# Performance work log

Measured on AMD Instinct MI355X. Metric: run time of the kernel, lower is better.

The kernel has to match this reference:

```python
import jax, jax.numpy as jnp
import numpy as np

N, E, G = 50000, 400000, 64   # nodes, edges, graphs
HEADS = 4
F_IN, H1, C3, OUT = 64, 96, 64, 10  # in feats, hidden (3*32), last conv out, classes


def seg_softmax(alpha, index, num_segments):
    # numerically stable softmax over segments (PyG softmax(alpha, edge_index_i))
    amax = jax.ops.segment_max(alpha, index, num_segments)
    amax = jnp.where(jnp.isfinite(amax), amax, 0.0)
    e = jnp.exp(alpha - amax[index])
    denom = jax.ops.segment_sum(e, index, num_segments)
    return e / (denom[index] + 1e-16)


def general_conv(x, src, dst, Wm, bm, att, Ws=None, bs=None):
    # GeneralConv (attention=True, additive, directed_msg, aggr='add')
    C = att.shape[-1]
    m = (x[src] @ Wm + bm).reshape(-1, HEADS, C)              # [E,H,C] gathered messages
    a = jax.nn.leaky_relu((m * att).sum(-1), 0.2)             # [E,H] attention logits
    a = seg_softmax(a, dst, N)                                # segment softmax per dest node
    agg = jax.ops.segment_sum(m * a[..., None], dst, N)       # [N,H,C] scatter-add
    out = agg.mean(axis=1)                                    # head mean -> [N,C]
    if Ws is None:                                            # lin_self = Identity (in==out)
        return out + x
    return out + x @ Ws + bs


def setup_inputs():
    key = jax.random.key(0)
    ks = jax.random.split(key, 16)
    s = 0.05
    return {
        "x": jax.random.normal(ks[0], (N, F_IN), jnp.float32),
        "edge_index": jax.random.randint(ks[1], (2, E), 0, N, jnp.int32),
        "batch": jnp.sort(jax.random.randint(ks[2], (N,), 0, G, jnp.int32)),
        # layer 1: F_IN -> H1
        "Wm1": jax.random.normal(ks[3], (F_IN, HEADS * H1), jnp.float32) * s,
        "bm1": jnp.zeros((HEADS * H1,), jnp.float32),
        "att1": jax.random.normal(ks[4], (HEADS, H1), jnp.float32) * s,
        "Ws1": jax.random.normal(ks[5], (F_IN, H1), jnp.float32) * s,
        "bs1": jnp.zeros((H1,), jnp.float32),
        # layer 2: H1 -> H1 (lin_self = Identity)
        "Wm2": jax.random.normal(ks[6], (H1, HEADS * H1), jnp.float32) * s,
        "bm2": jnp.zeros((HEADS * H1,), jnp.float32),
        "att2": jax.random.normal(ks[7], (HEADS, H1), jnp.float32) * s,
        # layer 3: H1 -> C3
        "Wm3": jax.random.normal(ks[8], (H1, HEADS * C3), jnp.float32) * s,
        "bm3": jnp.zeros((HEADS * C3,), jnp.float32),
        "att3": jax.random.normal(ks[9], (HEADS, C3), jnp.float32) * s,
        "Ws3": jax.random.normal(ks[10], (H1, C3), jnp.float32) * s,
        "bs3": jnp.zeros((C3,), jnp.float32),
        # classifier
        "Wfc": jax.random.normal(ks[11], (C3, OUT), jnp.float32) * s,
        "bfc": jnp.zeros((OUT,), jnp.float32),
    }


def reference(x, edge_index, batch, Wm1, bm1, att1, Ws1, bs1,
              Wm2, bm2, att2, Wm3, bm3, att3, Ws3, bs3, Wfc, bfc):
    src, dst = edge_index[0], edge_index[1]
    h = general_conv(x, src, dst, Wm1, bm1, att1, Ws1, bs1)
    h = general_conv(h, src, dst, Wm2, bm2, att2)
    h = general_conv(h, src, dst, Wm3, bm3, att3, Ws3, bs3)
    # global_mean_pool
    ssum = jax.ops.segment_sum(h, batch, G)
    cnt = jax.ops.segment_sum(jnp.ones((N, 1), h.dtype), batch, G)
    pooled = ssum / jnp.maximum(cnt, 1.0)                      # [G,C3]
    logits = pooled @ Wfc + bfc
    return jax.nn.log_softmax(logits, axis=1)
```

## Files before the change

kernel.cpp:

```cpp
#include <hip/hip_runtime.h>
#include <hip/hip_bf16.h>
#include <stdint.h>

using bf16 = __hip_bfloat16;
typedef __attribute__((ext_vector_type(8))) short bf16x8;
typedef __attribute__((ext_vector_type(4))) float f32x4;
typedef __attribute__((ext_vector_type(2))) float f32x2;

#define NN 50000
#define NE 400000
#define NG 64
#define FIN 64
#define HID 96
#define CC3 64
#define NOUT 10

#define SCAN_BLOCK 256
#define NPART ((NN + SCAN_BLOCK - 1) / SCAN_BLOCK)
#define PBW ((112*384 + 112*512 + 64*512)/256)
#define ELB ((NN/16 + 3)/4)

__device__ __forceinline__ float b2f(bf16 h){ return __bfloat162float(h); }
__device__ __forceinline__ bf16 f2b(float f){ return __float2bfloat16(f); }
__device__ __forceinline__ float blo(unsigned v){ return __uint_as_float(v << 16); }
__device__ __forceinline__ float bhi(unsigned v){ return __uint_as_float(v & 0xFFFF0000u); }

struct PrepA {
  const float *Wm1,*att1,*bm1,*Wm2,*att2,*bm2,*Wm3,*att3,*bm3,*bs1;
  float *f2,*f3,*lbv,*zb; bf16* WTf1;
  int* deg; float* psum; int* done;
};
__global__ __launch_bounds__(256) void prep_a_kernel(PrepA j){
  int bid = blockIdx.x;
  if (bid == 0){
    for (int i=threadIdx.x; i<96*4; i+=256){
      int k=i>>2, h=i&3; float a=0.f;
      for (int c=0;c<96;++c) a += j.Wm2[k*384 + h*96 + c]*j.att2[h*96+c];
      j.f2[i]=a;
    }
    for (int i=threadIdx.x; i<96*4; i+=256){
      int k=i>>2, h=i&3; float a=0.f;
      for (int c=0;c<64;++c) a += j.Wm3[k*256 + h*64 + c]*j.att3[h*64+c];
      j.f3[i]=a;
    }
    for (int i=threadIdx.x; i<16*64; i+=256){
      int col=i>>6, k=i&63; float a=0.f;
      if (col<4){ for (int c=0;c<96;++c) a += j.Wm1[k*384 + col*96 + c]*j.att1[col*96+c]; }
      j.WTf1[i] = f2b(a);
    }
    if (threadIdx.x < 96) j.zb[threadIdx.x] = 0.f;
    __syncthreads();
    if (threadIdx.x < 4){
      int h = threadIdx.x;
      float l1=0.f,l2=0.f,l3=0.f;
      for (int c=0;c<96;++c) l1 += j.bm1[h*96+c]*j.att1[h*96+c];
      for (int c=0;c<96;++c) l2 += j.bm2[h*96+c]*j.att2[h*96+c];
      for (int c=0;c<64;++c) l3 += j.bm3[h*64+c]*j.att3[h*64+c];
      float e2 = l2;
      for (int k=0;k<96;++k) e2 += j.bs1[k]*j.f2[k*4+h];
      j.lbv[h]=l1; j.lbv[4+h]=e2; j.lbv[8+h]=l3;
    }
  } else if (bid <= NPART){
    int i=(bid-1)*256+threadIdx.x;
    if (i<NN) j.deg[i]=0;
  } else {
    for (int i=threadIdx.x; i<NG*CC3; i+=256) j.psum[i]=0.f;
    if (threadIdx.x==0) *j.done = 0;
  }
}

struct PrepB {
  const float *Wm1,*bm1,*Ws1,*Wm2,*bm2,*Wm3,*bm3,*Ws3;
  const float *f2,*f3;
  bf16 *WT1,*WT2,*WT3;
  const float* x; const bf16* WTf1; const float* lbv;
  bf16* xb; uint8_t* x8; float* EL;
};
__device__ __forceinline__ float w1full(const PrepB& j, int k, int c){
  if (k < 256) return 0.25f*j.Wm1[(k&63)*384 + (k>>6)*96 + c];
  if (k == 256) return 0.25f*(j.bm1[c]+j.bm1[96+c]+j.bm1[192+c]+j.bm1[288+c]);
  if (k < 288) return 0.f;
  return j.Ws1[(k-288)*96 + c];
}
__device__ __forceinline__ float w2full(const PrepB& j, int k, int c){
  if (k < 384){ int kk=k%96, h=k/96; return 0.25f*j.Wm2[kk*384 + h*96 + c]; }
  if (k == 384) return 0.25f*(j.bm2[c]+j.bm2[96+c]+j.bm2[192+c]+j.bm2[288+c]);
  if (k < 416) return 0.f;
  return (k-416==c) ? 1.f : 0.f;
}
__device__ __forceinline__ float w3full(const PrepB& j, int k, int c){
  if (k < 384){ int kk=k%96, h=k/96; return 0.25f*j.Wm3[kk*256 + h*64 + c]; }
  if (k == 384) return 0.25f*(j.bm3[c]+j.bm3[64+c]+j.bm3[128+c]+j.bm3[192+c]);
  if (k < 416) return 0.f;
  return j.Ws3[(k-416)*64 + c];
}
__global__ __launch_bounds__(256) void prep_b_kernel(PrepB j){
  const int bid = blockIdx.x;
  if (bid < PBW){
    int idx = bid*256 + threadIdx.x;
    if (idx < 112*384){
      int col = idx/384, k = idx - col*384;
      float v;
      if (k >= 352) v = 0.f;
      else if (col < 96) v = w1full(j,k,col);
      else if (col < 100){ int h=col-96; float a=0.f;
        for (int c=0;c<96;++c) a += w1full(j,k,c)*j.f2[c*4+h]; v=a; }
      else v = 0.f;
      j.WT1[col*384 + k] = f2b(v);
    } else if (idx < 112*384 + 112*512){
      int r = idx - 112*384;
      int col = r/512, k = r - col*512;
      float v;
      if (col < 96) v = w2full(j,k,col);
      else if (col < 100){ int h=col-96; float a=0.f;
        for (int c=0;c<96;++c) a += w2full(j,k,c)*j.f3[c*4+h]; v=a; }
      else v = 0.f;
      j.WT2[col*512 + k] = f2b(v);
    } else {
      int r = idx - 112*384 - 112*512;
      int col = r/512, k = r - col*512;
      j.WT3[col*512 + k] = f2b(w3full(j,k,col));
    }
  } else {
    const int wave = threadIdx.x>>6, lane = threadIdx.x&63;
    const int tile = (bid - PBW)*4 + wave;
    if (tile >= NN/16) return;
    const int lm = lane&15, q = lane>>4;
    const size_t row = (size_t)tile*16 + lm;
    bf16x8 xf[2];
    #pragma unroll
    for (int kt=0;kt<2;++kt){
      float4 a0 = *(const float4*)(j.x + row*64 + kt*32 + q*8);
      float4 a1 = *(const float4*)(j.x + row*64 + kt*32 + q*8 + 4);
      bf16 t[8] = {f2b(a0.x),f2b(a0.y),f2b(a0.z),f2b(a0.w),
                   f2b(a1.x),f2b(a1.y),f2b(a1.z),f2b(a1.w)};
      xf[kt] = *(const bf16x8*)t;
      *(bf16x8*)(j.xb + row*64 + kt*32 + q*8) = xf[kt];
      int p0 = 0, p1 = 0;
      p0 = __builtin_amdgcn_cvt_pk_fp8_f32(a0.x, a0.y, p0, false);
      p0 = __builtin_amdgcn_cvt_pk_fp8_f32(a0.z, a0.w, p0, true);
      p1 = __builtin_amdgcn_cvt_pk_fp8_f32(a1.x, a1.y, p1, false);
      p1 = __builtin_amdgcn_cvt_pk_fp8_f32(a1.z, a1.w, p1, true);
      uint2 pk; pk.x = (unsigned)p0; pk.y = (unsigned)p1;
      *(uint2*)(j.x8 + row*64 + kt*32 + q*8) = pk;
    }
    f32x4 acc = {};
    #pragma unroll
    for (int kt=0;kt<2;++kt){
      bf16x8 wf = *(const bf16x8*)(j.WTf1 + (size_t)lm*64 + kt*32 + q*8);
      acc = __builtin_amdgcn_mfma_f32_16x16x32_bf16(wf, xf[kt], acc, 0,0,0);
    }
    if (q==0){
      float4 e; float l;
      l=acc[0]+j.lbv[0]; l=(l>=0.f)?l:0.2f*l; e.x=__expf(fminf(fmaxf(l,-60.f),60.f));
      l=acc[1]+j.lbv[1]; l=(l>=0.f)?l:0.2f*l; e.y=__expf(fminf(fmaxf(l,-60.f),60.f));
      l=acc[2]+j.lbv[2]; l=(l>=0.f)?l:0.2f*l; e.z=__expf(fminf(fmaxf(l,-60.f),60.f));
      l=acc[3]+j.lbv[3]; l=(l>=0.f)?l:0.2f*l; e.w=__expf(fminf(fmaxf(l,-60.f),60.f));
      *(float4*)(j.EL + 4*row) = e;
    }
  }
}

__global__ void deg_kernel(const int* __restrict__ ei, int* __restrict__ deg){
  int e = blockIdx.x*256 + threadIdx.x;
  if (e < NE) atomicAdd(&deg[ei[NE + e]], 1);
}

__global__ __launch_bounds__(256) void scan_part_kernel(const int* __restrict__ deg,
    int* __restrict__ partials, int* __restrict__ done, int* __restrict__ off){
  __shared__ int ws[4];
  __shared__ int lastflag;
  __shared__ int buf[256];
  int i = blockIdx.x*SCAN_BLOCK + threadIdx.x;
  int v = (i < NN) ? deg[i] : 0;
  int lane = threadIdx.x & 63, w = threadIdx.x >> 6;
  int s = v;
  #pragma unroll
  for (int m=1;m<64;m<<=1) s += __shfl_xor(s,m);
  if (lane==0) ws[w]=s;
  __syncthreads();
  if (threadIdx.x==0){
    int tot = ws[0]+ws[1]+ws[2]+ws[3];
    atomicExch(&partials[blockIdx.x], tot);
    __threadfence();
    int old = atomicAdd(done, 1);
    lastflag = (old == NPART-1) ? 1 : 0;
  }
  __syncthreads();
  if (lastflag){
    int t = threadIdx.x;
    int pv = (t < NPART) ? atomicAdd(&partials[t], 0) : 0;
    buf[t] = pv; __syncthreads();
    for (int st=1; st<256; st<<=1){
      int x = (t>=st) ? buf[t-st] : 0;
      __syncthreads();
      buf[t] += x;
      __syncthreads();
    }
    if (t < NPART) atomicExch(&partials[t], buf[t] - pv);
    if (t == 0) off[NN] = buf[255];
  }
}

__global__ __launch_bounds__(256) void scan_final_kernel(const int* __restrict__ deg,
    const int* __restrict__ partials, int* __restrict__ off, int* __restrict__ cursor){
  __shared__ int buf[256];
  int i = blockIdx.x*SCAN_BLOCK + threadIdx.x;
  int t = threadIdx.x;
  int v = (i<NN) ? deg[i] : 0;
  buf[t] = v; __syncthreads();
  for (int s=1;s<256;s<<=1){
    int x = (t>=s) ? buf[t-s] : 0;
    __syncthreads();
    buf[t] += x;
    __syncthreads();
  }
  int ex = partials[blockIdx.x] + buf[t] - v;
  if (i<NN){ off[i]=ex; cursor[i]=ex; }
}

__global__ void scatter_kernel(const int* __restrict__ ei, int* __restrict__ cursor,
                               int* __restrict__ csr_src){
  int e = blockIdx.x*256 + threadIdx.x;
  if (e < NE){
    int d = ei[NE + e];
    int slot = atomicAdd(&cursor[d], 1);
    csr_src[slot] = ei[e];
  }
}

template<int KH>
__global__ __launch_bounds__(256) void agg_kernel(
    const int* __restrict__ off, const int* __restrict__ csr_src,
    const float* __restrict__ ELin, const uint8_t* __restrict__ T8,
    bf16* __restrict__ Sb)
{
  constexpr int R  = 4*KH;
  constexpr int KS = R + 32;
  const int wave = threadIdx.x >> 6, lane = threadIdx.x & 63;
  const int n = blockIdx.x*4 + wave;
  const int e0 = off[n], e1 = off[n+1];

  if (KH == 64){
    const int hidx = lane >> 4;
    const int kk = (4*lane) & 63;
    float acc[4] = {0.f,0.f,0.f,0.f};
    float dnl = 0.f;
    int base = e0;
    int cnt  = min(8, e1-base);
    int sreg = (base < e1 && lane < cnt) ? csr_src[base+lane] : 0;
    while (base < e1){
      const int nbase = base + 8;
      const int ncnt  = min(8, e1-nbase);
      int nreg = (nbase < e1 && lane < ncnt) ? csr_src[nbase+lane] : 0;
      int sv[8];
      #pragma unroll
      for (int j=0;j<8;++j) sv[j] = __shfl(sreg, j);
      float wl[8]; unsigned u[8];
      #pragma unroll
      for (int j=0;j<8;++j){
        wl[j] = ELin[4*(size_t)sv[j] + hidx];
        u[j]  = *(const unsigned*)(T8 + (size_t)sv[j]*64 + kk);
      }
      #pragma unroll
      for (int j=0;j<8;++j){
        float w = (j < cnt) ? wl[j] : 0.f;
        dnl += w;
        f32x2 a0 = __builtin_amdgcn_cvt_pk_f32_fp8((int)u[j], false);
        f32x2 a1 = __builtin_amdgcn_cvt_pk_f32_fp8((int)u[j], true);
        acc[0] += a0.x*w;  acc[1] += a0.y*w;
        acc[2] += a1.x*w;  acc[3] += a1.y*w;
      }
      sreg = nreg; cnt = ncnt; base = nbase;
    }
    const float rd = 1.f/(dnl + 1e-16f);
    bf16* srow = Sb + (size_t)n*KS;
    bf16 st[4] = {f2b(acc[0]*rd), f2b(acc[1]*rd), f2b(acc[2]*rd), f2b(acc[3]*rd)};
    *(uint2*)(srow + hidx*64 + kk) = *(const uint2*)st;
    if (lane < 8){
      uint2 z; z.x = 0u; z.y = 0u;
      if (lane == 0 && e1 > e0) z.x = 0x3F80u;
      *(uint2*)(srow + R + lane*4) = z;
    }
  } else {
    const bool act = (8*lane) < R;
    const int hidx = min(3, (8*lane)/KH);
    const int kk = (8*lane) % KH;
    float acc[8] = {0.f,0.f,0.f,0.f,0.f,0.f,0.f,0.f};
    float dnl = 0.f;
    int base = e0;
    int cnt  = min(8, e1-base);
    int sreg = (base < e1 && lane < cnt) ? csr_src[base+lane] : 0;
    while (base < e1){
      const int nbase = base + 8;
      const int ncnt  = min(8, e1-nbase);
      int nreg = (nbase < e1 && lane < ncnt) ? csr_src[nbase+lane] : 0;
      int sv[8];
      #pragma unroll
      for (int j=0;j<8;++j) sv[j] = __shfl(sreg, j);
      float wl[8]; uint2 u[8];
      #pragma unroll
      for (int j=0;j<8;++j){
        wl[j] = ELin[4*(size_t)sv[j] + hidx];
        u[j]  = *(const uint2*)(T8 + (size_t)sv[j]*KH + kk);
      }
      #pragma unroll
      for (int j=0;j<8;++j){
        float w = (j < cnt) ? wl[j] : 0.f;
        dnl += w;
        f32x2 a0 = __builtin_amdgcn_cvt_pk_f32_fp8((int)u[j].x, false);
        f32x2 a1 = __builtin_amdgcn_cvt_pk_f32_fp8((int)u[j].x, true);
        f32x2 a2 = __builtin_amdgcn_cvt_pk_f32_fp8((int)u[j].y, false);
        f32x2 a3 = __builtin_amdgcn_cvt_pk_f32_fp8((int)u[j].y, true);
        acc[0] += a0.x*w;  acc[1] += a0.y*w;
        acc[2] += a1.x*w;  acc[3] += a1.y*w;
        acc[4] += a2.x*w;  acc[5] += a2.y*w;
        acc[6] += a3.x*w;  acc[7] += a3.y*w;
      }
      sreg = nreg; cnt = ncnt; base = nbase;
    }
    const float rd = 1.f/(dnl + 1e-16f);
    bf16* srow = Sb + (size_t)n*KS;
    if (act){
      bf16 st[8];
      #pragma unroll
      for (int t=0;t<8;++t) st[t] = f2b(acc[t]*rd);
      *(bf16x8*)(srow + 8*lane) = *(const bf16x8*)st;
    } else if (8*lane < KS){
      bf16 st[8] = {};
      if (8*lane == R) st[0] = f2b((e1 > e0) ? 1.f : 0.f);
      *(bf16x8*)(srow + 8*lane) = *(const bf16x8*)st;
    }
  }
}

template<int KH, int NCT, bool POOL>
__global__ __launch_bounds__(256, 3) void gemm_kernel(
    const bf16* __restrict__ Sb, const bf16* __restrict__ Hprev,
    const bf16* __restrict__ WT, const float* __restrict__ bias,
    const float* __restrict__ lbe, bf16* __restrict__ Hout,
    uint8_t* __restrict__ H8out, float* __restrict__ ELout,
    const int* __restrict__ batch, float* __restrict__ psum)
{
  constexpr int R      = 4*KH;
  constexpr int KS     = R + 32;
  constexpr int KA     = KS + KH;
  constexpr int KTS    = KS/32;
  constexpr int NKT    = KA/32;
  constexpr int NCHUNK = (NKT + 3)/4;
  constexpr int KAP    = NCHUNK*128;
  constexpr int NCOL   = NCT*16;
  constexpr int NT     = NN/16;
  constexpr int WSZ    = NCOL*256;
  constexpr int OSZ    = POOL ? (4*16*68*4) : (4*16*104*2);
  constexpr int USZ    = (WSZ > OSZ) ? WSZ : OSZ;
  __shared__ __align__(16) unsigned char lds[USZ];

  const int tid  = threadIdx.x;
  const int wave = tid >> 6, lane = tid & 63;
  const int lm = lane & 15, q = lane >> 4;
  const int tile = blockIdx.x*4 + wave;
  const bool active = (tile < NT);
  const int ctile = active ? tile : (NT-1);
  const size_t row = (size_t)ctile*16 + lm;

  const bf16* arow = Sb + row*KS;
  const bf16* hrow = Hprev + row*KH;
  const unsigned sw = (unsigned)((lm & 7) << 4);

  bf16x8 a[NKT];
  #pragma unroll
  for (int kt=0; kt<KTS; ++kt) a[kt] = *(const bf16x8*)(arow + kt*32 + q*8);
  #pragma unroll
  for (int kt=KTS; kt<NKT; ++kt) a[kt] = *(const bf16x8*)(hrow + (kt-KTS)*32 + q*8);

  f32x4 acc[NCT];
  #pragma unroll
  for (int c=0;c<NCT;++c) acc[c] = (f32x4){0.f,0.f,0.f,0.f};

  #pragma unroll
  for (int chunk=0; chunk<NCHUNK; ++chunk){
    if (chunk) __syncthreads();
    {
      const int k0 = chunk*128;
      #pragma unroll
      for (int it=0; it<NCOL*16/256; ++it){
        const int idx = it*256 + tid;
        const int col = idx >> 4, sg = idx & 15;
        uint4 v = *(const uint4*)(WT + (size_t)col*KAP + k0 + sg*8);
        const unsigned off = (unsigned)(sg*16) ^ (unsigned)((col & 7) << 4);
        *(uint4*)(lds + col*256 + off) = v;
      }
    }
    __syncthreads();
    #pragma unroll
    for (int ct=0; ct<NCT; ++ct){
      const unsigned char* rbase = lds + (ct*16 + lm)*256;
      #pragma unroll
      for (int t=0;t<4;++t){
        const int kt = chunk*4 + t;
        if (kt < NKT){
          bf16x8 wf = *(const bf16x8*)(rbase + (((unsigned)(t*64 + q*16)) ^ sw));
          acc[ct] = __builtin_amdgcn_mfma_f32_16x16x32_bf16(wf, a[kt], acc[ct], 0,0,0);
        }
      }
    }
  }
  __syncthreads();

  if (active){
    if (!POOL){
      unsigned short* ob = (unsigned short*)(lds) + wave*16*104;
      #pragma unroll
      for (int ct=0; ct<NCT-1; ++ct){
        const int c = ct*16 + q*4;
        bf16 st[4] = {f2b(acc[ct][0]+bias[c]),   f2b(acc[ct][1]+bias[c+1]),
                      f2b(acc[ct][2]+bias[c+2]), f2b(acc[ct][3]+bias[c+3])};
        *(uint2*)(ob + lm*104 + c) = *(const uint2*)st;
      }
      if (q == 0){
        float4 e; float l;
        l=acc[NCT-1][0]+lbe[0]; l=(l>=0.f)?l:0.2f*l; e.x=__expf(fminf(fmaxf(l,-60.f),60.f));
        l=acc[NCT-1][1]+lbe[1]; l=(l>=0.f)?l:0.2f*l; e.y=__expf(fminf(fmaxf(l,-60.f),60.f));
        l=acc[NCT-1][2]+lbe[2]; l=(l>=0.f)?l:0.2f*l; e.z=__expf(fminf(fmaxf(l,-60.f),60.f));
        l=acc[NCT-1][3]+lbe[3]; l=(l>=0.f)?l:0.2f*l; e.w=__expf(fminf(fmaxf(l,-60.f),60.f));
        *(float4*)(ELout + 4*row) = e;
      }
      __builtin_amdgcn_wave_barrier();
      const size_t n0w = (size_t)tile*16;
      #pragma unroll
      for (int jj=0; jj<3; ++jj){
        const int idx = jj*64 + lane;
        const int r = idx/12, ch = idx - r*12;
        uint4 v = *(const uint4*)(ob + r*104 + ch*8);
        *(uint4*)(Hout + (n0w+r)*96 + ch*8) = v;
        int p0 = 0, p1 = 0;
        p0 = __builtin_amdgcn_cvt_pk_fp8_f32(blo(v.x), bhi(v.x), p0, false);
        p0 = __builtin_amdgcn_cvt_pk_fp8_f32(blo(v.y), bhi(v.y), p0, true);
        p1 = __builtin_amdgcn_cvt_pk_fp8_f32(blo(v.z), bhi(v.z), p1, false);
        p1 = __builtin_amdgcn_cvt_pk_fp8_f32(blo(v.w), bhi(v.w), p1, true);
        uint2 pk; pk.x = (unsigned)p0; pk.y = (unsigned)p1;
        *(uint2*)(H8out + (n0w+r)*96 + ch*8) = pk;
      }
    } else {
      float* ob = (float*)(lds) + wave*16*68;
      #pragma unroll
      for (int ct=0; ct<NCT; ++ct){
        const int c = ct*16 + q*4;
        float* orow = ob + lm*68;
        orow[c]   = acc[ct][0]+bias[c];   orow[c+1] = acc[ct][1]+bias[c+1];
        orow[c+2] = acc[ct][2]+bias[c+2]; orow[c+3] = acc[ct][3]+bias[c+3];
      }
      int bload = (lane < 16) ? batch[tile*16 + lane] : 0;
      __builtin_amdgcn_wave_barrier();
      const int c = lane;
      int curg = __shfl(bload, 0); float a2 = 0.f;
      #pragma unroll
      for (int i=0;i<16;++i){
        float v = ob[i*68 + c];
        int g = __shfl(bload, i);
        if (g != curg){ atomicAdd(&psum[curg*64+c], a2); a2=0.f; curg=g; }
        a2 += v;
      }
      atomicAdd(&psum[curg*64+c], a2);
    }
  }
}

__global__ __launch_bounds__(64) void fc_kernel(const float* __restrict__ psum,
    const int* __restrict__ batch, const float* __restrict__ Wfc,
    const float* __restrict__ bfc, float* __restrict__ out){
  int g = blockIdx.x, t = threadIdx.x;
  __shared__ int sb[2];
  if (t < 2){
    int target = g + t;
    int lo=0, hi=NN;
    while (lo<hi){ int mid=(lo+hi)>>1; if (batch[mid]<target) lo=mid+1; else hi=mid; }
    sb[t]=lo;
  }
  __syncthreads();
  float cnt = (float)(sb[1]-sb[0]);
  __shared__ float p[CC3];
  __shared__ float lg[NOUT];
  p[t] = psum[g*CC3 + t] / fmaxf(cnt, 1.0f);
  __syncthreads();
  if (t < NOUT){
    float a = bfc[t];
    for (int c=0;c<CC3;++c) a += p[c]*Wfc[c*NOUT + t];
    lg[t] = a;
  }
  __syncthreads();
  if (t < NOUT){
    float m = -INFINITY;
    #pragma unroll
    for (int i=0;i<NOUT;++i) m = fmaxf(m, lg[i]);
    float s = 0.f;
    #pragma unroll
    for (int i=0;i<NOUT;++i) s += __expf(lg[i]-m);
    out[g*NOUT + t] = lg[t] - m - __logf(s);
  }
}

extern "C" void kernel_launch(void* const* d_in, const int* in_sizes, int n_in,
                              void* d_out, int out_size, void* d_ws, size_t ws_size,
                              hipStream_t stream) {
  const float* xf    = (const float*)d_in[0];
  const int*   ei    = (const int*)d_in[1];
  const int*   batch = (const int*)d_in[2];
  const float* pWm1  = (const float*)d_in[3];
  const float* pbm1  = (const float*)d_in[4];
  const float* patt1 = (const float*)d_in[5];
  const float* pWs1  = (const float*)d_in[6];
  const float* pbs1  = (const float*)d_in[7];
  const float* pWm2  = (const float*)d_in[8];
  const float* pbm2  = (const float*)d_in[9];
  const float* patt2 = (const float*)d_in[10];
  const float* pWm3  = (const float*)d_in[11];
  const float* pbm3  = (const float*)d_in[12];
  const float* patt3 = (const float*)d_in[13];
  const float* pWs3  = (const float*)d_in[14];
  const float* pbs3  = (const float*)d_in[15];
  const float* pWfc  = (const float*)d_in[16];
  const float* pbfc  = (const float*)d_in[17];

  char* p = (char*)d_ws;
  auto alloc = [&](size_t bytes)->char*{ char* q = p; p += (bytes + 255) & ~(size_t)255; return q; };
  int*     deg     = (int*)  alloc(NN*sizeof(int));
  int*     off     = (int*)  alloc((NN+1)*sizeof(int));
  int*     cursor  = (int*)  alloc(NN*sizeof(int));
  int*     csr_src = (int*)  alloc(NE*sizeof(int));
  int*     partials= (int*)  alloc(NPART*sizeof(int));
  int*     done    = (int*)  alloc(sizeof(int));
  float*   ELa     = (float*)alloc((size_t)NN*4*sizeof(float));
  float*   ELb     = (float*)alloc((size_t)NN*4*sizeof(float));
  bf16*    xb      = (bf16*) alloc((size_t)NN*64*sizeof(bf16));
  uint8_t* x8      = (uint8_t*)alloc((size_t)NN*64);
  uint8_t* H8      = (uint8_t*)alloc((size_t)NN*96);
  bf16*    H1b     = (bf16*) alloc((size_t)NN*96*sizeof(bf16));
  bf16*    H2b     = (bf16*) alloc((size_t)NN*96*sizeof(bf16));
  bf16*    Sb      = (bf16*) alloc((size_t)NN*416*sizeof(bf16));
  float*   psum    = (float*)alloc((size_t)NG*CC3*sizeof(float));
  float*   f2      = (float*)alloc(96*4*sizeof(float));
  float*   f3      = (float*)alloc(96*4*sizeof(float));
  float*   lbv     = (float*)alloc(12*sizeof(float));
  float*   zb      = (float*)alloc(96*sizeof(float));
  bf16*    WTf1    = (bf16*) alloc((size_t)16*64*sizeof(bf16));
  bf16*    WT1     = (bf16*) alloc((size_t)112*384*sizeof(bf16));
  bf16*    WT2     = (bf16*) alloc((size_t)112*512*sizeof(bf16));
  bf16*    WT3     = (bf16*) alloc((size_t)64*512*sizeof(bf16));

  PrepA pa;
  pa.Wm1=pWm1; pa.att1=patt1; pa.bm1=pbm1;
  pa.Wm2=pWm2; pa.att2=patt2; pa.bm2=pbm2;
  pa.Wm3=pWm3; pa.att3=patt3; pa.bm3=pbm3;
  pa.bs1=pbs1; pa.f2=f2; pa.f3=f3; pa.lbv=lbv; pa.zb=zb; pa.WTf1=WTf1;
  pa.deg=deg; pa.psum=psum; pa.done=done;
  prep_a_kernel<<<NPART+2, 256, 0, stream>>>(pa);

  PrepB pb;
  pb.Wm1=pWm1; pb.bm1=pbm1; pb.Ws1=pWs1;
  pb.Wm2=pWm2; pb.bm2=pbm2;
  pb.Wm3=pWm3; pb.bm3=pbm3; pb.Ws3=pWs3;
  pb.f2=f2; pb.f3=f3; pb.WT1=WT1; pb.WT2=WT2; pb.WT3=WT3;
  pb.x=xf; pb.WTf1=WTf1; pb.lbv=lbv; pb.xb=xb; pb.x8=x8; pb.EL=ELa;
  prep_b_kernel<<<PBW + ELB, 256, 0, stream>>>(pb);

  deg_kernel<<<(NE+255)/256, 256, 0, stream>>>(ei, deg);
  scan_part_kernel<<<NPART, 256, 0, stream>>>(deg, partials, done, off);
  scan_final_kernel<<<NPART, 256, 0, stream>>>(deg, partials, off, cursor);
  scatter_kernel<<<(NE+255)/256, 256, 0, stream>>>(ei, cursor, csr_src);

  const int AGB = NN/4;
  const int GGB = (NN/16 + 3)/4;

  agg_kernel<64><<<AGB, 256, 0, stream>>>(off, csr_src, ELa, x8, Sb);
  gemm_kernel<64,7,false><<<GGB, 256, 0, stream>>>(Sb, xb, WT1, pbs1, lbv+4,
                                                   H1b, H8, ELb, batch, psum);
  agg_kernel<96><<<AGB, 256, 0, stream>>>(off, csr_src, ELb, H8, Sb);
  gemm_kernel<96,7,false><<<GGB, 256, 0, stream>>>(Sb, H1b, WT2, zb, lbv+8,
                                                   H2b, H8, ELa, batch, psum);
  agg_kernel<96><<<AGB, 256, 0, stream>>>(off, csr_src, ELa, H8, Sb);
  gemm_kernel<96,4,true ><<<GGB, 256, 0, stream>>>(Sb, H2b, WT3, pbs3, nullptr,
                                                   nullptr, nullptr, nullptr, batch, psum);

  fc_kernel<<<NG, 64, 0, stream>>>(psum, batch, pWfc, pbfc, (float*)d_out);
}
```

Baseline: 326.6 us.

## Fuse degree count and CSR scatter into neighbours, pre-swizzle weights for direct LDS loads

The degree-count atomics are folded into the prep_b launch. The CSR scatter is merged into the final scan kernel through a grid-wide spin barrier on a new counter. Together these remove two kernel launches. The GEMM weight tensors are now written in pre-swizzled chunk-major layout, so the GEMM can stage them into LDS with global_load_lds instead of loading through registers and storing. The grid barrier assumes all NPART (196) blocks are co-resident, which holds on this GPU but is fragile.

```diff
diff --git a/kernel.cpp b/kernel.cpp
--- a/kernel.cpp
+++ b/kernel.cpp
@@ -19,16 +19,23 @@
 #define NPART ((NN + SCAN_BLOCK - 1) / SCAN_BLOCK)
 #define PBW ((112*384 + 112*512 + 64*512)/256)
 #define ELB ((NN/16 + 3)/4)
+#define DEGB ((NE + 255)/256)
 
 __device__ __forceinline__ float b2f(bf16 h){ return __bfloat162float(h); }
 __device__ __forceinline__ bf16 f2b(float f){ return __float2bfloat16(f); }
 __device__ __forceinline__ float blo(unsigned v){ return __uint_as_float(v << 16); }
 __device__ __forceinline__ float bhi(unsigned v){ return __uint_as_float(v & 0xFFFF0000u); }
 
+__device__ __forceinline__ size_t swzidx(int col, int k, int ncol){
+  int chunk = k >> 7, kr = k & 127, sg = kr >> 3, b = kr & 7;
+  unsigned byteoff = (unsigned)(sg*16) ^ (unsigned)((col & 7) << 4);
+  return (size_t)chunk*ncol*128 + (size_t)col*128 + (byteoff >> 1) + b;
+}
+
 struct PrepA {
   const float *Wm1,*att1,*bm1,*Wm2,*att2,*bm2,*Wm3,*att3,*bm3,*bs1;
   float *f2,*f3,*lbv,*zb; bf16* WTf1;
-  int* deg; float* psum; int* done;
+  int* deg; float* psum; int* done; int* done2;
 };
 __global__ __launch_bounds__(256) void prep_a_kernel(PrepA j){
   int bid = blockIdx.x;
@@ -65,7 +72,7 @@
     if (i<NN) j.deg[i]=0;
   } else {
     for (int i=threadIdx.x; i<NG*CC3; i+=256) j.psum[i]=0.f;
-    if (threadIdx.x==0) *j.done = 0;
+    if (threadIdx.x==0){ *j.done = 0; *j.done2 = 0; }
   }
 }
 
@@ -75,6 +82,7 @@
   bf16 *WT1,*WT2,*WT3;
   const float* x; const bf16* WTf1; const float* lbv;
   bf16* xb; uint8_t* x8; float* EL;
+  const int* ei; int* deg;
 };
 __device__ __forceinline__ float w1full(const PrepB& j, int k, int c){
   if (k < 256) return 0.25f*j.Wm1[(k&63)*384 + (k>>6)*96 + c];
@@ -106,7 +114,7 @@
       else if (col < 100){ int h=col-96; float a=0.f;
         for (int c=0;c<96;++c) a += w1full(j,k,c)*j.f2[c*4+h]; v=a; }
       else v = 0.f;
-      j.WT1[col*384 + k] = f2b(v);
+      j.WT1[swzidx(col,k,112)] = f2b(v);
     } else if (idx < 112*384 + 112*512){
       int r = idx - 112*384;
       int col = r/512, k = r - col*512;
@@ -115,13 +123,13 @@
       else if (col < 100){ int h=col-96; float a=0.f;
         for (int c=0;c<96;++c) a += w2full(j,k,c)*j.f3[c*4+h]; v=a; }
       else v = 0.f;
-      j.WT2[col*512 + k] = f2b(v);
+      j.WT2[swzidx(col,k,112)] = f2b(v);
     } else {
       int r = idx - 112*384 - 112*512;
       int col = r/512, k = r - col*512;
-      j.WT3[col*512 + k] = f2b(w3full(j,k,col));
-    }
-  } else {
+      j.WT3[swzidx(col,k,64)] = f2b(w3full(j,k,col));
+    }
+  } else if (bid < PBW + ELB){
     const int wave = threadIdx.x>>6, lane = threadIdx.x&63;
     const int tile = (bid - PBW)*4 + wave;
     if (tile >= NN/16) return;
@@ -158,12 +166,10 @@
       l=acc[3]+j.lbv[3]; l=(l>=0.f)?l:0.2f*l; e.w=__expf(fminf(fmaxf(l,-60.f),60.f));
       *(float4*)(j.EL + 4*row) = e;
     }
-  }
-}
-
-__global__ void deg_kernel(const int* __restrict__ ei, int* __restrict__ deg){
-  int e = blockIdx.x*256 + threadIdx.x;
-  if (e < NE) atomicAdd(&deg[ei[NE + e]], 1);
+  } else {
+    int e = (bid - PBW - ELB)*256 + threadIdx.x;
+    if (e < NE) atomicAdd(&j.deg[j.ei[NE + e]], 1);
+  }
 }
 
 __global__ __launch_bounds__(256) void scan_part_kernel(const int* __restrict__ deg,
@@ -202,8 +208,10 @@
   }
 }
 
-__global__ __launch_bounds__(256) void scan_final_kernel(const int* __restrict__ deg,
-    const int* __restrict__ partials, int* __restrict__ off, int* __restrict__ cursor){
+__global__ __launch_bounds__(256) void scan_final_scatter_kernel(
+    const int* __restrict__ deg, const int* __restrict__ partials,
+    int* __restrict__ off, int* __restrict__ cursor,
+    const int* __restrict__ ei, int* __restrict__ csr_src, int* __restrict__ done2){
   __shared__ int buf[256];
   int i = blockIdx.x*SCAN_BLOCK + threadIdx.x;
   int t = threadIdx.x;
@@ -217,12 +225,14 @@
   }
   int ex = partials[blockIdx.x] + buf[t] - v;
   if (i<NN){ off[i]=ex; cursor[i]=ex; }
-}
-
-__global__ void scatter_kernel(const int* __restrict__ ei, int* __restrict__ cursor,
-                               int* __restrict__ csr_src){
-  int e = blockIdx.x*256 + threadIdx.x;
-  if (e < NE){
+  __threadfence();
+  __syncthreads();
+  if (t==0){
+    atomicAdd(done2, 1);
+    while (atomicAdd(done2, 0) < NPART) __builtin_amdgcn_s_sleep(8);
+  }
+  __syncthreads();
+  for (int e = blockIdx.x*256 + t; e < NE; e += NPART*256){
     int d = ei[NE + e];
     int slot = atomicAdd(&cursor[d], 1);
     csr_src[slot] = ei[e];
@@ -348,7 +358,6 @@
   constexpr int KTS    = KS/32;
   constexpr int NKT    = KA/32;
   constexpr int NCHUNK = (NKT + 3)/4;
-  constexpr int KAP    = NCHUNK*128;
   constexpr int NCOL   = NCT*16;
   constexpr int NT     = NN/16;
   constexpr int WSZ    = NCOL*256;
@@ -382,14 +391,14 @@
   for (int chunk=0; chunk<NCHUNK; ++chunk){
     if (chunk) __syncthreads();
     {
-      const int k0 = chunk*128;
-      #pragma unroll
-      for (int it=0; it<NCOL*16/256; ++it){
-        const int idx = it*256 + tid;
-        const int col = idx >> 4, sg = idx & 15;
-        uint4 v = *(const uint4*)(WT + (size_t)col*KAP + k0 + sg*8);
-        const unsigned off = (unsigned)(sg*16) ^ (unsigned)((col & 7) << 4);
-        *(uint4*)(lds + col*256 + off) = v;
+      const char* wbase = (const char*)WT + (size_t)chunk*NCOL*256;
+      #pragma unroll
+      for (int it=0; it<WSZ/4096; ++it){
+        const unsigned boff = (unsigned)(it*4096 + tid*16);
+        __builtin_amdgcn_global_load_lds(
+            (const __attribute__((address_space(1))) uint32_t*)(wbase + boff),
+            (__attribute__((address_space(3))) uint32_t*)(lds + boff),
+            16, 0, 0);
       }
     }
     __syncthreads();
@@ -531,6 +540,7 @@
   int*     csr_src = (int*)  alloc(NE*sizeof(int));
   int*     partials= (int*)  alloc(NPART*sizeof(int));
   int*     done    = (int*)  alloc(sizeof(int));
+  int*     done2   = (int*)  alloc(sizeof(int));
   float*   ELa     = (float*)alloc((size_t)NN*4*sizeof(float));
   float*   ELb     = (float*)alloc((size_t)NN*4*sizeof(float));
   bf16*    xb      = (bf16*) alloc((size_t)NN*64*sizeof(bf16));
@@ -554,7 +564,7 @@
   pa.Wm2=pWm2; pa.att2=patt2; pa.bm2=pbm2;
   pa.Wm3=pWm3; pa.att3=patt3; pa.bm3=pbm3;
   pa.bs1=pbs1; pa.f2=f2; pa.f3=f3; pa.lbv=lbv; pa.zb=zb; pa.WTf1=WTf1;
-  pa.deg=deg; pa.psum=psum; pa.done=done;
+  pa.deg=deg; pa.psum=psum; pa.done=done; pa.done2=done2;
   prep_a_kernel<<<NPART+2, 256, 0, stream>>>(pa);
 
   PrepB pb;
@@ -563,12 +573,12 @@
   pb.Wm3=pWm3; pb.bm3=pbm3; pb.Ws3=pWs3;
   pb.f2=f2; pb.f3=f3; pb.WT1=WT1; pb.WT2=WT2; pb.WT3=WT3;
   pb.x=xf; pb.WTf1=WTf1; pb.lbv=lbv; pb.xb=xb; pb.x8=x8; pb.EL=ELa;
-  prep_b_kernel<<<PBW + ELB, 256, 0, stream>>>(pb);
-
-  deg_kernel<<<(NE+255)/256, 256, 0, stream>>>(ei, deg);
+  pb.ei=ei; pb.deg=deg;
+  prep_b_kernel<<<PBW + ELB + DEGB, 256, 0, stream>>>(pb);
+
   scan_part_kernel<<<NPART, 256, 0, stream>>>(deg, partials, done, off);
-  scan_final_kernel<<<NPART, 256, 0, stream>>>(deg, partials, off, cursor);
-  scatter_kernel<<<(NE+255)/256, 256, 0, stream>>>(ei, cursor, csr_src);
+  scan_final_scatter_kernel<<<NPART, 256, 0, stream>>>(deg, partials, off, cursor,
+                                                       ei, csr_src, done2);
 
   const int AGB = NN/4;
   const int GGB = (NN/16 + 3)/4;
```

Result: slower. 340.7 us (+4.3%).
